# Optimization experiments

Measured on AMD Instinct MI355X. Metric: run time of the kernel, lower is better.

Reference implementation:

```python
import jax, jax.numpy as jnp
import numpy as np
import math

K = 10      # number of propagation steps
BETA = 2.0  # log-weighting base
N_NODES = 100000
N_EDGES = 1000000
HIDDEN = 64


def setup_inputs() -> dict:
    key = jax.random.key(0)
    k1, k2, k3 = jax.random.split(key, 3)
    feat = jax.random.normal(k1, (N_NODES, HIDDEN), dtype=jnp.float32)
    src = jax.random.randint(k2, (N_EDGES,), 0, N_NODES, dtype=jnp.int64)
    dst = jax.random.randint(k3, (N_EDGES,), 0, N_NODES, dtype=jnp.int64)
    return {"feat": feat, "src": src, "dst": dst}


def reference(feat, src, dst):
    n = feat.shape[0]
    ones_e = jnp.ones(src.shape, dtype=feat.dtype)
    # out-degree of source nodes, in-degree of destination nodes
    out_deg = jax.ops.segment_sum(ones_e, src, num_segments=n)
    in_deg = jax.ops.segment_sum(ones_e, dst, num_segments=n)
    src_norm = jnp.maximum(out_deg, 1.0) ** -0.5  # [N]
    dst_norm = jnp.maximum(in_deg, 1.0) ** -0.5   # [N]

    # log-based combination weights over the K+1 snapshots
    logs = [math.log(BETA + i) for i in range(1, K + 2)]
    denom = sum(logs)
    w = [l / denom for l in logs]

    h = feat
    out = w[0] * feat
    for step in range(K):
        # gather-scale on source side, scatter-sum to destinations, scale on dst side
        m = (h * src_norm[:, None])[src]                      # [E, D]
        h = jax.ops.segment_sum(m, dst, num_segments=n)       # [N, D]
        h = h * dst_norm[:, None]
        out = out + w[step + 1] * h
    return out
```

## Files before the change

### kernel.cpp

```cpp
#include <hip/hip_runtime.h>
#include <hip/hip_bf16.h>
#include <math.h>

#define HIDDEN 64
#define K_STEPS 10
#define FULLN 102400
#define FULLW (FULLN / 4)
#define PADU 4

struct Wts { float v[K_STEPS + 1]; };

typedef float v2f __attribute__((ext_vector_type(2)));

__device__ __forceinline__ float bits2f(unsigned int u) {
    union { unsigned int i; float f; } c; c.i = u; return c.f;
}
__device__ __forceinline__ unsigned short f2bf(float f) {
    union { float f; unsigned int u; } c; c.f = f;
    unsigned int u = c.u;
    return (unsigned short)((u + 0x7FFF + ((u >> 16) & 1)) >> 16);
}
__device__ __forceinline__ void unpack_add(v2f acc[4], uint4 v) {
    v2f t;
    t.x = bits2f(v.x << 16); t.y = bits2f(v.x & 0xFFFF0000u); acc[0] += t;
    t.x = bits2f(v.y << 16); t.y = bits2f(v.y & 0xFFFF0000u); acc[1] += t;
    t.x = bits2f(v.z << 16); t.y = bits2f(v.z & 0xFFFF0000u); acc[2] += t;
    t.x = bits2f(v.w << 16); t.y = bits2f(v.w & 0xFFFF0000u); acc[3] += t;
}

__global__ void detect_kernel(const int* __restrict__ srcw,
                              const unsigned short* __restrict__ featw,
                              int* __restrict__ flags) {
    __shared__ int odd_nonzero;
    __shared__ int exp_in_range;
    if (threadIdx.x == 0) { odd_nonzero = 0; exp_in_range = 0; }
    __syncthreads();
    int w = srcw[2 * threadIdx.x + 1];
    if (w != 0) atomicAdd(&odd_nonzero, 1);
    unsigned short f = featw[2 * threadIdx.x];
    int ex = (f >> 7) & 0xFF;
    if (ex >= 90 && ex <= 135) atomicAdd(&exp_in_range, 1);
    __syncthreads();
    if (threadIdx.x == 0) {
        flags[0] = (odd_nonzero == 0) ? 1 : 0;
        flags[1] = (exp_in_range >= 240) ? 0 : 1;
    }
}

__global__ __launch_bounds__(1024) void hist_kernel(
        const void* __restrict__ src, const void* __restrict__ dst,
        const int* __restrict__ flags,
        unsigned* __restrict__ partials,
        unsigned char* __restrict__ rank,
        int E, int chunkE, int nchunks) {
    __shared__ unsigned bins[FULLW];
    int cx = blockIdx.x, az = blockIdx.y;
    for (int i = threadIdx.x; i < FULLW; i += 1024) bins[i] = 0;
    __syncthreads();
    const void* arr = az ? dst : src;
    int i64 = flags[0];
    int base = cx * chunkE;
    int lim = min(base + chunkE, E);
    for (int e = base + threadIdx.x; e < lim; e += 1024) {
        int v = i64 ? (int)((const long long*)arr)[e] : ((const int*)arr)[e];
        unsigned uv = (unsigned)v;
        int sh = (uv & 3) * 8;
        unsigned old = atomicAdd(&bins[uv >> 2], 1u << sh);
        if (az) rank[e] = (unsigned char)((old >> sh) & 0xFF);
    }
    __syncthreads();
    unsigned* out = partials + ((size_t)(az * nchunks + cx)) * FULLW;
    for (int i = threadIdx.x; i < FULLW; i += 1024) out[i] = bins[i];
}

__global__ void reduce_kernel(const unsigned* __restrict__ partials,
                              unsigned* __restrict__ chunk_pre,
                              int* __restrict__ out_deg, int* __restrict__ in_deg,
                              float* __restrict__ src_norm, float* __restrict__ dst_norm,
                              int N, int nchunks) {
    int t = blockIdx.x * blockDim.x + threadIdx.x;
    if (t >= 2 * FULLW) return;
    int a = t / FULLW;
    int lw = t % FULLW;
    const unsigned* p = partials + ((size_t)a * nchunks) * FULLW + lw;
    unsigned sum = 0;
    if (a == 1) {
        for (int c = 0; c < nchunks; ++c) {
            chunk_pre[(size_t)c * FULLW + lw] = sum;
            sum += p[(size_t)c * FULLW];
        }
    } else {
        for (int c = 0; c < nchunks; ++c) sum += p[(size_t)c * FULLW];
    }
    int nodeBase = lw * 4;
    int* deg = a ? in_deg : out_deg;
    float* nrm = a ? dst_norm : src_norm;
    #pragma unroll
    for (int k = 0; k < 4; ++k) {
        int n = nodeBase + k;
        if (n < N) {
            int d = (int)((sum >> (k * 8)) & 0xFF);
            deg[n] = d;
            nrm[n] = 1.0f / sqrtf(fmaxf((float)d, 1.0f));
        }
    }
}

__global__ void scanA_kernel(const int* __restrict__ deg, int* __restrict__ row_ptr,
                             int* __restrict__ block_sums, int N) {
    __shared__ int lds[256];
    int t = threadIdx.x;
    int base = blockIdx.x * 1024 + t * 4;
    int v0 = (base + 0 < N) ? ((deg[base + 0] + (PADU - 1)) & ~(PADU - 1)) : 0;
    int v1 = (base + 1 < N) ? ((deg[base + 1] + (PADU - 1)) & ~(PADU - 1)) : 0;
    int v2 = (base + 2 < N) ? ((deg[base + 2] + (PADU - 1)) & ~(PADU - 1)) : 0;
    int v3 = (base + 3 < N) ? ((deg[base + 3] + (PADU - 1)) & ~(PADU - 1)) : 0;
    int s = v0 + v1 + v2 + v3;
    lds[t] = s;
    __syncthreads();
    for (int off = 1; off < 256; off <<= 1) {
        int x = 0;
        if (t >= off) x = lds[t - off];
        __syncthreads();
        if (t >= off) lds[t] += x;
        __syncthreads();
    }
    int excl = lds[t] - s;
    if (t == 255) block_sums[blockIdx.x] = lds[255];
    if (base + 0 < N) row_ptr[base + 0] = excl;
    if (base + 1 < N) row_ptr[base + 1] = excl + v0;
    if (base + 2 < N) row_ptr[base + 2] = excl + v0 + v1;
    if (base + 3 < N) row_ptr[base + 3] = excl + v0 + v1 + v2;
}

__global__ void scanB_kernel(int* __restrict__ bs, int nb) {
    __shared__ int lds[1024];
    int t = threadIdx.x;
    int v = (t < nb) ? bs[t] : 0;
    lds[t] = v;
    __syncthreads();
    for (int off = 1; off < 1024; off <<= 1) {
        int x = 0;
        if (t >= off) x = lds[t - off];
        __syncthreads();
        if (t >= off) lds[t] += x;
        __syncthreads();
    }
    if (t < nb) bs[t] = lds[t] - v;
    if (t == nb - 1) bs[1024] = lds[t];
}

__global__ void scanC_pad_kernel(const int* __restrict__ raw_row,
                                 const int* __restrict__ block_offs,
                                 const int* __restrict__ in_deg,
                                 int* __restrict__ row_fin,
                                 int* __restrict__ col, int N) {
    int i = blockIdx.x * blockDim.x + threadIdx.x;
    if (i >= N) return;
    int b0 = raw_row[i] + block_offs[i >> 10];
    int b1 = (i + 1 < N) ? (raw_row[i + 1] + block_offs[(i + 1) >> 10])
                         : block_offs[1024];
    row_fin[i] = b0;
    if (i == 0) row_fin[N] = block_offs[1024];
    int s = b0 + in_deg[i];
    for (int j = s; j < b1; ++j) col[j] = N;
}

__global__ void scatter_kernel(const void* __restrict__ src, const void* __restrict__ dst,
                               const int* __restrict__ flags,
                               const int* __restrict__ row_fin,
                               const unsigned* __restrict__ chunk_pre,
                               const unsigned char* __restrict__ rank,
                               int* __restrict__ col, int E, int chunkShift) {
    int i64 = flags[0];
    int stride = gridDim.x * blockDim.x;
    for (int e = blockIdx.x * blockDim.x + threadIdx.x; e < E; e += stride) {
        int s, d;
        if (i64) { s = (int)((const long long*)src)[e]; d = (int)((const long long*)dst)[e]; }
        else     { s = ((const int*)src)[e];            d = ((const int*)dst)[e]; }
        int c = e >> chunkShift;
        unsigned prew = chunk_pre[(size_t)c * FULLW + ((unsigned)d >> 2)];
        int pre = (int)((prew >> ((d & 3) * 8)) & 0xFF);
        col[row_fin[d] + pre + (int)rank[e]] = s;
    }
}

__global__ void init_kernel(const void* __restrict__ feat_raw,
                            const int* __restrict__ flags,
                            const float* __restrict__ src_norm,
                            uint4* __restrict__ hs8, float4* __restrict__ out_acc4,
                            float w0, int nchunks, int writeAcc,
                            int snapN, int nsnap) {
    int i = blockIdx.x * blockDim.x + threadIdx.x;
    if (i >= nchunks) {
        int j = i - nchunks;
        int k = j >> 3, r = j & 7;
        if (k < nsnap) {
            uint4 z; z.x = 0u; z.y = 0u; z.z = 0u; z.w = 0u;
            hs8[(size_t)k * snapN + nchunks + r] = z;
        }
        return;
    }
    int n = i >> 3;
    int c = i & 7;
    float sn = src_norm[n];
    float f[8];
    if (flags[1]) {
        float4 a = ((const float4*)feat_raw)[i * 2];
        float4 b = ((const float4*)feat_raw)[i * 2 + 1];
        f[0] = a.x; f[1] = a.y; f[2] = a.z; f[3] = a.w;
        f[4] = b.x; f[5] = b.y; f[6] = b.z; f[7] = b.w;
    } else {
        uint4 u = ((const uint4*)feat_raw)[i];
        f[0] = bits2f(u.x << 16); f[1] = bits2f(u.x & 0xFFFF0000u);
        f[2] = bits2f(u.y << 16); f[3] = bits2f(u.y & 0xFFFF0000u);
        f[4] = bits2f(u.z << 16); f[5] = bits2f(u.z & 0xFFFF0000u);
        f[6] = bits2f(u.w << 16); f[7] = bits2f(u.w & 0xFFFF0000u);
    }
    uint4 h;
    h.x = (unsigned int)f2bf(f[0] * sn) | ((unsigned int)f2bf(f[1] * sn) << 16);
    h.y = (unsigned int)f2bf(f[2] * sn) | ((unsigned int)f2bf(f[3] * sn) << 16);
    h.z = (unsigned int)f2bf(f[4] * sn) | ((unsigned int)f2bf(f[5] * sn) << 16);
    h.w = (unsigned int)f2bf(f[6] * sn) | ((unsigned int)f2bf(f[7] * sn) << 16);
    hs8[i] = h;
    if (writeAcc) {
        float4 o0, o1;
        o0.x = w0 * f[0]; o0.y = w0 * f[1]; o0.z = w0 * f[2]; o0.w = w0 * f[3];
        o1.x = w0 * f[4]; o1.y = w0 * f[5]; o1.z = w0 * f[6]; o1.w = w0 * f[7];
        size_t ob = (size_t)n * 16 + c * 2;
        out_acc4[ob] = o0;
        out_acc4[ob + 1] = o1;
    }
}

__device__ __forceinline__ void gather_row(const uint4* __restrict__ hs8,
                                           const int* __restrict__ col,
                                           int beg, int end, int fo,
                                           v2f a0[4], v2f a1[4]) {
    int e = beg;
    int nq = (end - beg) >> 2;
    if (nq & 1) {
        int4 c = *(const int4*)(col + e);
        uint4 v0 = hs8[((unsigned)c.x << 3) | fo];
        uint4 v1 = hs8[((unsigned)c.y << 3) | fo];
        uint4 v2 = hs8[((unsigned)c.z << 3) | fo];
        uint4 v3 = hs8[((unsigned)c.w << 3) | fo];
        unpack_add(a0, v0);
        unpack_add(a1, v1);
        unpack_add(a0, v2);
        unpack_add(a1, v3);
        e += 4;
    }
    if (e < end) {
        int4 c0 = *(const int4*)(col + e);
        int4 c1 = *(const int4*)(col + e + 4);
        for (;;) {
            int4 d0 = c0, d1 = c1;
            int ne = e + 8;
            if (ne < end) {
                c0 = *(const int4*)(col + ne);
                c1 = *(const int4*)(col + ne + 4);
            }
            uint4 v0 = hs8[((unsigned)d0.x << 3) | fo];
            uint4 v1 = hs8[((unsigned)d0.y << 3) | fo];
            uint4 v2 = hs8[((unsigned)d0.z << 3) | fo];
            uint4 v3 = hs8[((unsigned)d0.w << 3) | fo];
            uint4 v4 = hs8[((unsigned)d1.x << 3) | fo];
            uint4 v5 = hs8[((unsigned)d1.y << 3) | fo];
            uint4 v6 = hs8[((unsigned)d1.z << 3) | fo];
            uint4 v7 = hs8[((unsigned)d1.w << 3) | fo];
            unpack_add(a0, v0);
            unpack_add(a1, v1);
            unpack_add(a0, v2);
            unpack_add(a1, v3);
            unpack_add(a0, v4);
            unpack_add(a1, v5);
            unpack_add(a0, v6);
            unpack_add(a1, v7);
            e = ne;
            if (e >= end) break;
        }
    }
}

__global__ __launch_bounds__(256) void step_snap(
        const uint4* __restrict__ hs8, const int* __restrict__ row_fin,
        const int* __restrict__ col, const float* __restrict__ src_norm,
        const float* __restrict__ dst_norm, uint4* __restrict__ hs_next8, int N) {
    int wid = (blockIdx.x * 256 + threadIdx.x) >> 6;
    int nw = (gridDim.x * 256) >> 6;
    int lane = threadIdx.x & 63;
    int grp = lane >> 3, fo = lane & 7;
    for (int nbase = wid * 8; nbase < N; nbase += nw * 8) {
        int node = nbase + grp;
        int beg = 0, end = 0;
        if (node < N) { beg = row_fin[node]; end = row_fin[node + 1]; }
        v2f a0[4] = {v2f{0.f,0.f}, v2f{0.f,0.f}, v2f{0.f,0.f}, v2f{0.f,0.f}};
        v2f a1[4] = {v2f{0.f,0.f}, v2f{0.f,0.f}, v2f{0.f,0.f}, v2f{0.f,0.f}};
        if (beg < end) gather_row(hs8, col, beg, end, fo, a0, a1);
        if (node < N) {
            float m = dst_norm[node] * src_norm[node];
            #pragma unroll
            for (int k = 0; k < 4; ++k) a0[k] += a1[k];
            uint4 hn;
            hn.x = (unsigned int)f2bf(a0[0].x * m) | ((unsigned int)f2bf(a0[0].y * m) << 16);
            hn.y = (unsigned int)f2bf(a0[1].x * m) | ((unsigned int)f2bf(a0[1].y * m) << 16);
            hn.z = (unsigned int)f2bf(a0[2].x * m) | ((unsigned int)f2bf(a0[2].y * m) << 16);
            hn.w = (unsigned int)f2bf(a0[3].x * m) | ((unsigned int)f2bf(a0[3].y * m) << 16);
            hs_next8[((unsigned)node << 3) | fo] = hn;
        }
    }
}

template <bool LAST>
__global__ __launch_bounds__(256) void step_acc(
        const uint4* __restrict__ hs8, const int* __restrict__ row_fin,
        const int* __restrict__ col, const float* __restrict__ src_norm,
        const float* __restrict__ dst_norm, uint4* __restrict__ hs_next8,
        float4* __restrict__ out_acc4, float4* __restrict__ out4, float w, int N) {
    int wid = (blockIdx.x * 256 + threadIdx.x) >> 6;
    int nw = (gridDim.x * 256) >> 6;
    int lane = threadIdx.x & 63;
    int grp = lane >> 3, fo = lane & 7;
    for (int nbase = wid * 8; nbase < N; nbase += nw * 8) {
        int node = nbase + grp;
        int beg = 0, end = 0;
        if (node < N) { beg = row_fin[node]; end = row_fin[node + 1]; }
        v2f a0[4] = {v2f{0.f,0.f}, v2f{0.f,0.f}, v2f{0.f,0.f}, v2f{0.f,0.f}};
        v2f a1[4] = {v2f{0.f,0.f}, v2f{0.f,0.f}, v2f{0.f,0.f}, v2f{0.f,0.f}};
        if (beg < end) gather_row(hs8, col, beg, end, fo, a0, a1);
        if (node < N) {
            #pragma unroll
            for (int k = 0; k < 4; ++k) a0[k] += a1[k];
            float dn = dst_norm[node];
            float h0 = a0[0].x * dn, h1 = a0[0].y * dn, h2 = a0[1].x * dn, h3 = a0[1].y * dn;
            float h4 = a0[2].x * dn, h5 = a0[2].y * dn, h6 = a0[3].x * dn, h7 = a0[3].y * dn;
            size_t ob = (size_t)node * 16 + fo * 2;
            float4 o0 = out_acc4[ob];
            float4 o1 = out_acc4[ob + 1];
            o0.x += w * h0; o0.y += w * h1; o0.z += w * h2; o0.w += w * h3;
            o1.x += w * h4; o1.y += w * h5; o1.z += w * h6; o1.w += w * h7;
            if (LAST) {
                out4[ob] = o0;
                out4[ob + 1] = o1;
            } else {
                out_acc4[ob] = o0;
                out_acc4[ob + 1] = o1;
                float sn = src_norm[node];
                uint4 hn;
                hn.x = (unsigned int)f2bf(h0 * sn) | ((unsigned int)f2bf(h1 * sn) << 16);
                hn.y = (unsigned int)f2bf(h2 * sn) | ((unsigned int)f2bf(h3 * sn) << 16);
                hn.z = (unsigned int)f2bf(h4 * sn) | ((unsigned int)f2bf(h5 * sn) << 16);
                hn.w = (unsigned int)f2bf(h6 * sn) | ((unsigned int)f2bf(h7 * sn) << 16);
                hs_next8[((unsigned)node << 3) | fo] = hn;
            }
        }
    }
}

__global__ void combine_kernel(const void* __restrict__ feat_raw,
                               const int* __restrict__ flags,
                               const int* __restrict__ out_deg,
                               const uint4* __restrict__ hs_base,
                               float4* __restrict__ out4,
                               Wts wts, int snapN, int nchunks) {
    int i = blockIdx.x * blockDim.x + threadIdx.x;
    if (i >= nchunks) return;
    int n = i >> 3;
    float inv = sqrtf(fmaxf((float)out_deg[n], 1.0f));
    float acc[8];
    if (flags[1]) {
        float4 a = ((const float4*)feat_raw)[i * 2];
        float4 b = ((const float4*)feat_raw)[i * 2 + 1];
        acc[0] = a.x; acc[1] = a.y; acc[2] = a.z; acc[3] = a.w;
        acc[4] = b.x; acc[5] = b.y; acc[6] = b.z; acc[7] = b.w;
    } else {
        uint4 u = ((const uint4*)feat_raw)[i];
        acc[0] = bits2f(u.x << 16); acc[1] = bits2f(u.x & 0xFFFF0000u);
        acc[2] = bits2f(u.y << 16); acc[3] = bits2f(u.y & 0xFFFF0000u);
        acc[4] = bits2f(u.z << 16); acc[5] = bits2f(u.z & 0xFFFF0000u);
        acc[6] = bits2f(u.w << 16); acc[7] = bits2f(u.w & 0xFFFF0000u);
    }
    float w0 = wts.v[0];
    #pragma unroll
    for (int j = 0; j < 8; ++j) acc[j] *= w0;
    #pragma unroll
    for (int k = 1; k <= K_STEPS; ++k) {
        uint4 u = hs_base[(size_t)k * snapN + i];
        float s = wts.v[k] * inv;
        acc[0] += s * bits2f(u.x << 16); acc[1] += s * bits2f(u.x & 0xFFFF0000u);
        acc[2] += s * bits2f(u.y << 16); acc[3] += s * bits2f(u.y & 0xFFFF0000u);
        acc[4] += s * bits2f(u.z << 16); acc[5] += s * bits2f(u.z & 0xFFFF0000u);
        acc[6] += s * bits2f(u.w << 16); acc[7] += s * bits2f(u.w & 0xFFFF0000u);
    }
    float4 o0 = {acc[0], acc[1], acc[2], acc[3]};
    float4 o1 = {acc[4], acc[5], acc[6], acc[7]};
    out4[i * 2] = o0;
    out4[i * 2 + 1] = o1;
}

extern "C" void kernel_launch(void* const* d_in, const int* in_sizes, int n_in,
                              void* d_out, int out_size, void* d_ws, size_t ws_size,
                              hipStream_t stream) {
    const void* feat_raw = d_in[0];
    const void* src_raw = d_in[1];
    const void* dst_raw = d_in[2];
    float4* out4 = (float4*)d_out;

    const int N = in_sizes[0] / HIDDEN;
    const int E = (in_sizes[1] > 1500000) ? in_sizes[1] / 2 : in_sizes[1];
    const int nchunks = N * 8;
    const int snapN = nchunks + 8;
    const int Ecap = E + (PADU - 1) * N + 16;

    auto align256 = [](size_t b) { return (b + 255) & ~(size_t)255; };
    size_t base_bytes = align256(2 * sizeof(int))
                      + align256((size_t)N * sizeof(int))
                      + align256((size_t)N * sizeof(int))
                      + align256((size_t)(N + 1) * sizeof(int))
                      + align256((size_t)(N + 1) * sizeof(int))
                      + align256(1025 * sizeof(int))
                      + align256((size_t)Ecap * sizeof(int))
                      + align256((size_t)N * sizeof(float))
                      + align256((size_t)N * sizeof(float))
                      + align256((size_t)E);
    auto hist_bytes = [&](int C) {
        return align256((size_t)2 * C * FULLW * sizeof(unsigned))
             + align256((size_t)C * FULLW * sizeof(unsigned));
    };
    size_t snap_bytes = align256((size_t)(K_STEPS + 1) * snapN * sizeof(uint4));
    size_t acc_bytes  = align256((size_t)2 * snapN * sizeof(uint4))
                      + align256((size_t)N * 16 * sizeof(float4));

    int chunkShift = 13;
    int CHc = (E + (1 << chunkShift) - 1) >> chunkShift;
    int snapMode;
    if (ws_size >= base_bytes + hist_bytes(CHc) + snap_bytes) {
        snapMode = 1;
    } else {
        chunkShift = 14;
        CHc = (E + (1 << chunkShift) - 1) >> chunkShift;
        if (ws_size >= base_bytes + hist_bytes(CHc) + snap_bytes) {
            snapMode = 1;
        } else if (ws_size >= base_bytes + hist_bytes(CHc) + acc_bytes) {
            snapMode = 0;
        } else {
            chunkShift = 15;
            CHc = (E + (1 << chunkShift) - 1) >> chunkShift;
            snapMode = 0;
        }
    }
    const int chunkE = 1 << chunkShift;

    char* p = (char*)d_ws;
    auto alloc = [&](size_t bytes) {
        char* r = p;
        p += (bytes + 255) & ~(size_t)255;
        return r;
    };
    int* flags = (int*)alloc(2 * sizeof(int));
    int* out_deg = (int*)alloc((size_t)N * sizeof(int));
    int* in_deg = (int*)alloc((size_t)N * sizeof(int));
    int* row_ptr = (int*)alloc((size_t)(N + 1) * sizeof(int));
    int* row_fin = (int*)alloc((size_t)(N + 1) * sizeof(int));
    int* block_sums = (int*)alloc(1025 * sizeof(int));
    int* col = (int*)alloc((size_t)Ecap * sizeof(int));
    float* src_norm = (float*)alloc((size_t)N * sizeof(float));
    float* dst_norm = (float*)alloc((size_t)N * sizeof(float));
    unsigned char* rank = (unsigned char*)alloc((size_t)E);
    unsigned* partials = (unsigned*)alloc((size_t)2 * CHc * FULLW * sizeof(unsigned));
    unsigned* chunk_pre = (unsigned*)alloc((size_t)CHc * FULLW * sizeof(unsigned));
    uint4* hs_region;
    float4* out_acc = nullptr;
    if (snapMode) {
        hs_region = (uint4*)alloc((size_t)(K_STEPS + 1) * snapN * sizeof(uint4));
    } else {
        hs_region = (uint4*)alloc((size_t)2 * snapN * sizeof(uint4));
        out_acc = (float4*)alloc((size_t)N * 16 * sizeof(float4));
    }

    double logs[K_STEPS + 1];
    double denom = 0.0;
    for (int i = 0; i < K_STEPS + 1; ++i) {
        logs[i] = log(2.0 + (double)(i + 1));
        denom += logs[i];
    }
    Wts wts;
    for (int i = 0; i < K_STEPS + 1; ++i) wts.v[i] = (float)(logs[i] / denom);

    detect_kernel<<<1, 256, 0, stream>>>((const int*)src_raw,
                                         (const unsigned short*)feat_raw, flags);
    hist_kernel<<<dim3(CHc, 2), 1024, 0, stream>>>(src_raw, dst_raw, flags,
                                                   partials, rank, E, chunkE, CHc);
    reduce_kernel<<<(2 * FULLW + 255) / 256, 256, 0, stream>>>(
        partials, chunk_pre, out_deg, in_deg, src_norm, dst_norm, N, CHc);

    int nb = (N + 1023) / 1024;
    scanA_kernel<<<nb, 256, 0, stream>>>(in_deg, row_ptr, block_sums, N);
    scanB_kernel<<<1, 1024, 0, stream>>>(block_sums, nb);
    scanC_pad_kernel<<<(N + 255) / 256, 256, 0, stream>>>(row_ptr, block_sums, in_deg,
                                                          row_fin, col, N);
    scatter_kernel<<<min(2048, (E + 255) / 256), 256, 0, stream>>>(
        src_raw, dst_raw, flags, row_fin, chunk_pre, rank, col, E, chunkShift);

    const int nsnap = snapMode ? (K_STEPS + 1) : 2;
    init_kernel<<<(nchunks + nsnap * 8 + 255) / 256, 256, 0, stream>>>(
        feat_raw, flags, src_norm, hs_region, out_acc, wts.v[0], nchunks,
        snapMode ? 0 : 1, snapN, nsnap);

    const int work_blocks = (((N + 7) / 8) + 3) / 4;
    if (snapMode) {
        for (int step = 0; step < K_STEPS; ++step) {
            const uint4* cur = hs_region + (size_t)step * snapN;
            uint4* nxt = hs_region + (size_t)(step + 1) * snapN;
            step_snap<<<work_blocks, 256, 0, stream>>>(cur, row_fin, col, src_norm,
                                                       dst_norm, nxt, N);
        }
        combine_kernel<<<(nchunks + 255) / 256, 256, 0, stream>>>(
            feat_raw, flags, out_deg, hs_region, out4, wts, snapN, nchunks);
    } else {
        uint4* cur = hs_region;
        uint4* nxt = hs_region + snapN;
        for (int step = 0; step < K_STEPS; ++step) {
            if (step == K_STEPS - 1) {
                step_acc<true><<<work_blocks, 256, 0, stream>>>(
                    cur, row_fin, col, src_norm, dst_norm, nxt, out_acc, out4,
                    wts.v[step + 1], N);
            } else {
                step_acc<false><<<work_blocks, 256, 0, stream>>>(
                    cur, row_fin, col, src_norm, dst_norm, nxt, out_acc, out4,
                    wts.v[step + 1], N);
            }
            uint4* t = cur; cur = nxt; nxt = t;
        }
    }
}
```

Measured before the change: 376.7 us.

## Fuse final propagation step with combine; stage chunk prefixes in LDS for scatter

The last propagation step is merged with the weighted combine, so the final snapshot is never written to memory and read back, and one kernel launch is removed. The scatter kernel now runs one 1024-thread block per edge chunk and first copies that chunk's prefix table into shared memory, so the per-edge prefix lookups hit LDS instead of global memory. The cost is a roughly 100KB shared-memory load per block, which limits occupancy, and a combine tail that now runs inside the irregular gather kernel.

```diff
diff --git a/kernel.cpp b/kernel.cpp
--- a/kernel.cpp
+++ b/kernel.cpp
@@ -166,22 +166,28 @@
     for (int j = s; j < b1; ++j) col[j] = N;
 }
 
-__global__ void scatter_kernel(const void* __restrict__ src, const void* __restrict__ dst,
-                               const int* __restrict__ flags,
-                               const int* __restrict__ row_fin,
-                               const unsigned* __restrict__ chunk_pre,
-                               const unsigned char* __restrict__ rank,
-                               int* __restrict__ col, int E, int chunkShift) {
+__global__ __launch_bounds__(1024) void scatter_kernel(
+        const void* __restrict__ src, const void* __restrict__ dst,
+        const int* __restrict__ flags,
+        const int* __restrict__ row_fin,
+        const unsigned* __restrict__ chunk_pre,
+        const unsigned char* __restrict__ rank,
+        int* __restrict__ col, int E, int chunkE) {
+    __shared__ unsigned pre[FULLW];
+    int cx = blockIdx.x;
+    const unsigned* gpre = chunk_pre + (size_t)cx * FULLW;
+    for (int i = threadIdx.x; i < FULLW; i += 1024) pre[i] = gpre[i];
+    __syncthreads();
     int i64 = flags[0];
-    int stride = gridDim.x * blockDim.x;
-    for (int e = blockIdx.x * blockDim.x + threadIdx.x; e < E; e += stride) {
+    int base = cx * chunkE;
+    int lim = min(base + chunkE, E);
+    for (int e = base + threadIdx.x; e < lim; e += 1024) {
         int s, d;
         if (i64) { s = (int)((const long long*)src)[e]; d = (int)((const long long*)dst)[e]; }
         else     { s = ((const int*)src)[e];            d = ((const int*)dst)[e]; }
-        int c = e >> chunkShift;
-        unsigned prew = chunk_pre[(size_t)c * FULLW + ((unsigned)d >> 2)];
-        int pre = (int)((prew >> ((d & 3) * 8)) & 0xFF);
-        col[row_fin[d] + pre + (int)rank[e]] = s;
+        unsigned prew = pre[(unsigned)d >> 2];
+        int pr = (int)((prew >> ((d & 3) * 8)) & 0xFF);
+        col[row_fin[d] + pr + (int)rank[e]] = s;
     }
 }
 
@@ -308,6 +314,67 @@
             hn.z = (unsigned int)f2bf(a0[2].x * m) | ((unsigned int)f2bf(a0[2].y * m) << 16);
             hn.w = (unsigned int)f2bf(a0[3].x * m) | ((unsigned int)f2bf(a0[3].y * m) << 16);
             hs_next8[((unsigned)node << 3) | fo] = hn;
+        }
+    }
+}
+
+__global__ __launch_bounds__(256) void step_last(
+        const uint4* __restrict__ hs8, const int* __restrict__ row_fin,
+        const int* __restrict__ col, const float* __restrict__ dst_norm,
+        const void* __restrict__ feat_raw, const int* __restrict__ flags,
+        const int* __restrict__ out_deg, const uint4* __restrict__ hs_base,
+        float4* __restrict__ out4, Wts wts, int snapN, int N) {
+    int wid = (blockIdx.x * 256 + threadIdx.x) >> 6;
+    int nw = (gridDim.x * 256) >> 6;
+    int lane = threadIdx.x & 63;
+    int grp = lane >> 3, fo = lane & 7;
+    for (int nbase = wid * 8; nbase < N; nbase += nw * 8) {
+        int node = nbase + grp;
+        int beg = 0, end = 0;
+        if (node < N) { beg = row_fin[node]; end = row_fin[node + 1]; }
+        v2f a0[4] = {v2f{0.f,0.f}, v2f{0.f,0.f}, v2f{0.f,0.f}, v2f{0.f,0.f}};
+        v2f a1[4] = {v2f{0.f,0.f}, v2f{0.f,0.f}, v2f{0.f,0.f}, v2f{0.f,0.f}};
+        if (beg < end) gather_row(hs8, col, beg, end, fo, a0, a1);
+        if (node < N) {
+            float dn = dst_norm[node];
+            #pragma unroll
+            for (int k = 0; k < 4; ++k) a0[k] += a1[k];
+            int i = (node << 3) | fo;
+            float acc[8];
+            if (flags[1]) {
+                float4 a = ((const float4*)feat_raw)[i * 2];
+                float4 b = ((const float4*)feat_raw)[i * 2 + 1];
+                acc[0] = a.x; acc[1] = a.y; acc[2] = a.z; acc[3] = a.w;
+                acc[4] = b.x; acc[5] = b.y; acc[6] = b.z; acc[7] = b.w;
+            } else {
+                uint4 u = ((const uint4*)feat_raw)[i];
+                acc[0] = bits2f(u.x << 16); acc[1] = bits2f(u.x & 0xFFFF0000u);
+                acc[2] = bits2f(u.y << 16); acc[3] = bits2f(u.y & 0xFFFF0000u);
+                acc[4] = bits2f(u.z << 16); acc[5] = bits2f(u.z & 0xFFFF0000u);
+                acc[6] = bits2f(u.w << 16); acc[7] = bits2f(u.w & 0xFFFF0000u);
+            }
+            float w0 = wts.v[0];
+            #pragma unroll
+            for (int j = 0; j < 8; ++j) acc[j] *= w0;
+            float inv = sqrtf(fmaxf((float)out_deg[node], 1.0f));
+            #pragma unroll
+            for (int k = 1; k < K_STEPS; ++k) {
+                uint4 u = hs_base[(size_t)k * snapN + i];
+                float sc = wts.v[k] * inv;
+                acc[0] += sc * bits2f(u.x << 16); acc[1] += sc * bits2f(u.x & 0xFFFF0000u);
+                acc[2] += sc * bits2f(u.y << 16); acc[3] += sc * bits2f(u.y & 0xFFFF0000u);
+                acc[4] += sc * bits2f(u.z << 16); acc[5] += sc * bits2f(u.z & 0xFFFF0000u);
+                acc[6] += sc * bits2f(u.w << 16); acc[7] += sc * bits2f(u.w & 0xFFFF0000u);
+            }
+            float wK = wts.v[K_STEPS] * dn;
+            acc[0] += wK * a0[0].x; acc[1] += wK * a0[0].y;
+            acc[2] += wK * a0[1].x; acc[3] += wK * a0[1].y;
+            acc[4] += wK * a0[2].x; acc[5] += wK * a0[2].y;
+            acc[6] += wK * a0[3].x; acc[7] += wK * a0[3].y;
+            float4 o0 = {acc[0], acc[1], acc[2], acc[3]};
+            float4 o1 = {acc[4], acc[5], acc[6], acc[7]};
+            out4[i * 2] = o0;
+            out4[i * 2 + 1] = o1;
         }
     }
 }
@@ -358,47 +425,6 @@
     }
 }
 
-__global__ void combine_kernel(const void* __restrict__ feat_raw,
-                               const int* __restrict__ flags,
-                               const int* __restrict__ out_deg,
-                               const uint4* __restrict__ hs_base,
-                               float4* __restrict__ out4,
-                               Wts wts, int snapN, int nchunks) {
-    int i = blockIdx.x * blockDim.x + threadIdx.x;
-    if (i >= nchunks) return;
-    int n = i >> 3;
-    float inv = sqrtf(fmaxf((float)out_deg[n], 1.0f));
-    float acc[8];
-    if (flags[1]) {
-        float4 a = ((const float4*)feat_raw)[i * 2];
-        float4 b = ((const float4*)feat_raw)[i * 2 + 1];
-        acc[0] = a.x; acc[1] = a.y; acc[2] = a.z; acc[3] = a.w;
-        acc[4] = b.x; acc[5] = b.y; acc[6] = b.z; acc[7] = b.w;
-    } else {
-        uint4 u = ((const uint4*)feat_raw)[i];
-        acc[0] = bits2f(u.x << 16); acc[1] = bits2f(u.x & 0xFFFF0000u);
-        acc[2] = bits2f(u.y << 16); acc[3] = bits2f(u.y & 0xFFFF0000u);
-        acc[4] = bits2f(u.z << 16); acc[5] = bits2f(u.z & 0xFFFF0000u);
-        acc[6] = bits2f(u.w << 16); acc[7] = bits2f(u.w & 0xFFFF0000u);
-    }
-    float w0 = wts.v[0];
-    #pragma unroll
-    for (int j = 0; j < 8; ++j) acc[j] *= w0;
-    #pragma unroll
-    for (int k = 1; k <= K_STEPS; ++k) {
-        uint4 u = hs_base[(size_t)k * snapN + i];
-        float s = wts.v[k] * inv;
-        acc[0] += s * bits2f(u.x << 16); acc[1] += s * bits2f(u.x & 0xFFFF0000u);
-        acc[2] += s * bits2f(u.y << 16); acc[3] += s * bits2f(u.y & 0xFFFF0000u);
-        acc[4] += s * bits2f(u.z << 16); acc[5] += s * bits2f(u.z & 0xFFFF0000u);
-        acc[6] += s * bits2f(u.w << 16); acc[7] += s * bits2f(u.w & 0xFFFF0000u);
-    }
-    float4 o0 = {acc[0], acc[1], acc[2], acc[3]};
-    float4 o1 = {acc[4], acc[5], acc[6], acc[7]};
-    out4[i * 2] = o0;
-    out4[i * 2 + 1] = o1;
-}
-
 extern "C" void kernel_launch(void* const* d_in, const int* in_sizes, int n_in,
                               void* d_out, int out_size, void* d_ws, size_t ws_size,
                               hipStream_t stream) {
@@ -500,8 +526,8 @@
     scanB_kernel<<<1, 1024, 0, stream>>>(block_sums, nb);
     scanC_pad_kernel<<<(N + 255) / 256, 256, 0, stream>>>(row_ptr, block_sums, in_deg,
                                                           row_fin, col, N);
-    scatter_kernel<<<min(2048, (E + 255) / 256), 256, 0, stream>>>(
-        src_raw, dst_raw, flags, row_fin, chunk_pre, rank, col, E, chunkShift);
+    scatter_kernel<<<CHc, 1024, 0, stream>>>(src_raw, dst_raw, flags, row_fin,
+                                             chunk_pre, rank, col, E, chunkE);
 
     const int nsnap = snapMode ? (K_STEPS + 1) : 2;
     init_kernel<<<(nchunks + nsnap * 8 + 255) / 256, 256, 0, stream>>>(
@@ -510,14 +536,16 @@
 
     const int work_blocks = (((N + 7) / 8) + 3) / 4;
     if (snapMode) {
-        for (int step = 0; step < K_STEPS; ++step) {
+        for (int step = 0; step < K_STEPS - 1; ++step) {
             const uint4* cur = hs_region + (size_t)step * snapN;
             uint4* nxt = hs_region + (size_t)(step + 1) * snapN;
             step_snap<<<work_blocks, 256, 0, stream>>>(cur, row_fin, col, src_norm,
                                                        dst_norm, nxt, N);
         }
-        combine_kernel<<<(nchunks + 255) / 256, 256, 0, stream>>>(
-            feat_raw, flags, out_deg, hs_region, out4, wts, snapN, nchunks);
+        const uint4* last_in = hs_region + (size_t)(K_STEPS - 1) * snapN;
+        step_last<<<work_blocks, 256, 0, stream>>>(
+            last_in, row_fin, col, dst_norm, feat_raw, flags, out_deg,
+            hs_region, out4, wts, snapN, N);
     } else {
         uint4* cur = hs_region;
         uint4* nxt = hs_region + snapN;
```

Result: faster. 367.4 us (-2.5%).
